# Kernel tuning notes

Hardware: AMD Instinct MI355X
Metric: run time of the kernel (lower is better)

The kernel has to match this reference:

```python
import jax, jax.numpy as jnp
import numpy as np

D, H, L, NB = 128, 8, 2, 32
NEIGHBOR_DIST = 50.0
OUT_H, PRED = 512, 60
N, A, T = 32, 50, 50
DH = D // H
FF = 4 * D


def setup_inputs():
    key = jax.random.key(0)
    ks = jax.random.split(key, 20)
    g = lambda k, s, sc=0.02: jax.random.normal(k, s, jnp.float32) * sc
    return {
        "x": jax.random.normal(ks[0], (N, A, T, 5), jnp.float32) * 10.0,
        "invalid_entries": jax.random.randint(ks[1], (N, A, T), 0, 2).astype(bool),
        "emb_W": g(ks[2], (5, D)), "emb_b": jnp.zeros((D,), jnp.float32),
        "dist_emb": g(ks[3], (NB, H)),
        "ln_g": jnp.ones((L, 3, D), jnp.float32), "ln_b": jnp.zeros((L, 3, D), jnp.float32),
        "Wq": g(ks[4], (L, 2, D, D)), "Wk": g(ks[5], (L, 2, D, D)),
        "Wv": g(ks[6], (L, 2, D, D)), "Wo": g(ks[7], (L, 2, D, D)),
        "ffn_W1": g(ks[8], (L, D, FF)), "ffn_b1": jnp.zeros((L, FF), jnp.float32),
        "ffn_W2": g(ks[9], (L, FF, D)), "ffn_b2": jnp.zeros((L, D), jnp.float32),
        "mlp_W1": g(ks[10], (D, OUT_H)), "mlp_b1": jnp.zeros((OUT_H,), jnp.float32),
        "mlp_W2": g(ks[11], (OUT_H, 2 * PRED)), "mlp_b2": jnp.zeros((2 * PRED,), jnp.float32),
    }


def _ln(h, g, b):
    mu = h.mean(-1, keepdims=True)
    var = ((h - mu) ** 2).mean(-1, keepdims=True)
    return (h - mu) / jnp.sqrt(var + 1e-5) * g + b


def _mha(h, Wq, Wk, Wv, Wo, mask, bias=None):
    # h: (B, S, D); mask: (B, S, S) bool, True = blocked; bias: (B, H, S, S)
    B, S, _ = h.shape
    q = (h @ Wq).reshape(B, S, H, DH)
    k = (h @ Wk).reshape(B, S, H, DH)
    v = (h @ Wv).reshape(B, S, H, DH)
    s = jnp.einsum('bqhd,bkhd->bhqk', q, k) / jnp.sqrt(jnp.float32(DH))
    if bias is not None:
        s = s + bias
    s = jnp.where(mask[:, None, :, :], jnp.float32(-1e9), s)
    a = jax.nn.softmax(s, axis=-1)
    o = jnp.einsum('bhqk,bkhd->bqhd', a, v).reshape(B, S, D)
    return o @ Wo


def _masks_and_bias(x, invalid_entries, dist_emb):
    # pos: (N*T, A, 2); masks are non-differentiable, stop grad through cdist
    pos = jax.lax.stop_gradient(jnp.swapaxes(x, 1, 2).reshape(N * T, A, 5)[:, :, :2])
    dist = jnp.sqrt(jnp.sum((pos[:, :, None, :] - pos[:, None, :, :]) ** 2, axis=-1))
    bin_size = NEIGHBOR_DIST / NB
    bucket = jnp.clip((dist / bin_size).astype(jnp.int32), 0, NB - 1)
    dist_bias = jnp.transpose(dist_emb[bucket], (0, 3, 1, 2))  # (N*T, H, A, A)

    inv_s = jnp.swapaxes(invalid_entries, 1, 2).reshape(N * T, A)
    ego_only = jnp.ones((A, A), bool).at[0, :].set(False)  # only ego row attends broadly
    social = (dist > NEIGHBOR_DIST) | inv_s[:, None, :] | ego_only[None]
    di_a = jnp.arange(min(50, A))
    social = social.at[:, di_a, di_a].set(False)  # vectorized form of the 50-iter loop

    inv_t = invalid_entries.reshape(N * A, T)
    temporal = jnp.triu(jnp.ones((T, T), bool), 1)[None] | inv_t[:, None, :]
    di_t = jnp.arange(min(50, T))
    temporal = temporal.at[:, di_t, di_t].set(False)
    return temporal, social, dist_bias


def _forward(x, invalid_entries, emb_W, emb_b, dist_emb, ln_g, ln_b,
             Wq, Wk, Wv, Wo, ffn_W1, ffn_b1, ffn_W2, ffn_b2,
             mlp_W1, mlp_b1, mlp_W2, mlp_b2):
    temporal_mask, social_mask, dist_bias = _masks_and_bias(x, invalid_entries, dist_emb)
    h = x @ emb_W + emb_b  # (N, A, T, D)
    for l in range(L):
        # temporal attention over T per agent
        ht = h.reshape(N * A, T, D)
        ht = ht + _mha(_ln(ht, ln_g[l, 0], ln_b[l, 0]),
                       Wq[l, 0], Wk[l, 0], Wv[l, 0], Wo[l, 0], temporal_mask)
        h = ht.reshape(N, A, T, D)
        # social attention over A per timestep, with bucketized distance bias
        hs = jnp.swapaxes(h, 1, 2).reshape(N * T, A, D)
        hs = hs + _mha(_ln(hs, ln_g[l, 1], ln_b[l, 1]),
                       Wq[l, 1], Wk[l, 1], Wv[l, 1], Wo[l, 1], social_mask, bias=dist_bias)
        h = jnp.swapaxes(hs.reshape(N, T, A, D), 1, 2)
        # FFN
        hn = _ln(h, ln_g[l, 2], ln_b[l, 2])
        h = h + (jnp.maximum(hn @ ffn_W1[l] + ffn_b1[l], 0.0) @ ffn_W2[l] + ffn_b2[l])
    e = h[:, 0]  # ego agent: (N, T, D)
    e = (e @ mlp_W1 + mlp_b1) @ mlp_W2 + mlp_b2  # two linears, no activation (as in source)
    return e.reshape(N, T, PRED, 2)


def reference(x, invalid_entries, emb_W, emb_b, dist_emb, ln_g, ln_b,
              Wq, Wk, Wv, Wo, ffn_W1, ffn_b1, ffn_W2, ffn_b2,
              mlp_W1, mlp_b1, mlp_W2, mlp_b2):
    return _forward(x, invalid_entries, emb_W, emb_b, dist_emb, ln_g, ln_b,
                    Wq, Wk, Wv, Wo, ffn_W1, ffn_b1, ffn_W2, ffn_b2,
                    mlp_W1, mlp_b1, mlp_W2, mlp_b2)
```

## Files before the change

### kernel.cpp

```cpp
#include <hip/hip_runtime.h>


#define DD 128
typedef __attribute__((ext_vector_type(8))) short bf16x8;
typedef __attribute__((ext_vector_type(4))) float f32x4;
#define MFMA16(a, b, c) __builtin_amdgcn_mfma_f32_16x16x32_bf16(a, b, c, 0, 0, 0)

__device__ __forceinline__ float bf2f(unsigned short u) {
  union { unsigned int i; float f; } x; x.i = ((unsigned int)u) << 16; return x.f;
}
__device__ __forceinline__ unsigned short f2bf(float f) {
  union { float f; unsigned int i; } x; x.f = f;
  return (unsigned short)((x.i + 0x7FFFu + ((x.i >> 16) & 1u)) >> 16);
}
__device__ __forceinline__ float wave_sum(float v) {
#pragma unroll
  for (int off = 32; off > 0; off >>= 1) v += __shfl_xor(v, off, 64);
  return v;
}
__device__ __forceinline__ float wave_max(float v) {
#pragma unroll
  for (int off = 32; off > 0; off >>= 1) v = fmaxf(v, __shfl_xor(v, off, 64));
  return v;
}
__device__ __forceinline__ bool load_inv(const void* p, int idx, int bytemode) {
  if (bytemode) return ((const unsigned char*)p)[idx] != 0;
  return ((const int*)p)[idx] != 0;
}

__global__ void detect_kernel(const void* __restrict__ inv, int* __restrict__ flag) {
  __shared__ int found;
  if (threadIdx.x == 0) found = 0;
  __syncthreads();
  const unsigned char* p = (const unsigned char*)inv;
  int loc = 0;
  for (int i = threadIdx.x; i < 16384; i += blockDim.x)
    if ((i & 3) != 0 && p[i] != 0) loc = 1;
  if (loc) atomicOr(&found, 1);
  __syncthreads();
  if (threadIdx.x == 0) *flag = found ? 1 : 0;
}

__global__ __launch_bounds__(256) void convert_weights(
    const float* __restrict__ Wq, const float* __restrict__ Wk,
    const float* __restrict__ Wv, const float* __restrict__ Wo,
    const float* __restrict__ W1, const float* __restrict__ W2,
    const float* __restrict__ W1m, const float* __restrict__ W2m,
    unsigned short* __restrict__ wqkv, unsigned short* __restrict__ wot,
    unsigned short* __restrict__ w1t, unsigned short* __restrict__ w2t,
    unsigned short* __restrict__ w1e, unsigned short* __restrict__ w2e) {
  __shared__ float tile[32][33];
  int b = blockIdx.x;
  int tx = threadIdx.x & 31, ty = threadIdx.x >> 5;
  const float* src; unsigned short* dst;
  int o0, i0, srcld, dstld, osub = 0, obound = 1 << 30;
  if (b < 192) {
    int m = b / 48, t2 = b % 48;
    o0 = (t2 / 4) * 32; i0 = (t2 % 4) * 32;
    int sel = o0 >> 7;
    src = (sel == 0 ? Wq : (sel == 1 ? Wk : Wv)) + m * 16384;
    osub = sel * 128; srcld = 128;
    dst = wqkv + m * 49152; dstld = 128;
  } else if (b < 256) {
    int m = (b - 192) / 16, t2 = (b - 192) % 16;
    o0 = (t2 / 4) * 32; i0 = (t2 % 4) * 32;
    src = Wo + m * 16384; srcld = 128;
    dst = wot + m * 16384; dstld = 128;
  } else if (b < 384) {
    int l = (b - 256) / 64, t2 = (b - 256) % 64;
    o0 = (t2 / 4) * 32; i0 = (t2 % 4) * 32;
    src = W1 + l * 65536; srcld = 512;
    dst = w1t + l * 65536; dstld = 128;
  } else if (b < 512) {
    int l = (b - 384) / 64, t2 = (b - 384) % 64;
    o0 = (t2 / 16) * 32; i0 = (t2 % 16) * 32;
    src = W2 + l * 65536; srcld = 128;
    dst = w2t + l * 65536; dstld = 512;
  } else if (b < 576) {
    int t2 = b - 512;
    o0 = (t2 / 4) * 32; i0 = (t2 % 4) * 32;
    src = W1m; srcld = 512;
    dst = w1e; dstld = 128;
  } else {
    int t2 = b - 576;
    o0 = (t2 / 16) * 32; i0 = (t2 % 16) * 32;
    src = W2m; srcld = 120; obound = 120;
    dst = w2e; dstld = 512;
  }
#pragma unroll
  for (int kk = 0; kk < 4; ++kk) {
    int i = i0 + ty + 8 * kk, o = o0 + tx;
    tile[ty + 8 * kk][tx] = (o < obound) ? src[i * srcld + (o - osub)] : 0.f;
  }
  __syncthreads();
#pragma unroll
  for (int kk = 0; kk < 4; ++kk) {
    int o = o0 + ty + 8 * kk, i = i0 + tx;
    dst[o * dstld + i] = f2bf(tile[tx][ty + 8 * kk]);
  }
}

__global__ __launch_bounds__(512, 4) void temporal_attn_kernel(
    const float* __restrict__ x, float* __restrict__ h,
    const void* __restrict__ inv, const int* __restrict__ flagp,
    const float* __restrict__ g, const float* __restrict__ bb,
    const float* __restrict__ embW, const float* __restrict__ embB,
    const unsigned short* __restrict__ wqkv,
    const unsigned short* __restrict__ wot, int first) {
  __shared__ __align__(16) unsigned short xbf[64][136];
  __shared__ __align__(16) unsigned short kbf[64][136];
  __shared__ __align__(16) unsigned short vT[128][72];
  __shared__ __align__(16) unsigned short pbuf[8][16][72];
  __shared__ float ssb[8][64];
  int seq = blockIdx.x;
  int tid = threadIdx.x, lane = tid & 63, wid = tid >> 6;
  unsigned long long invmask =
      __ballot((lane < 50) && load_inv(inv, seq * 50 + lane, *flagp));
  const f32x4 zf = (f32x4){0.f, 0.f, 0.f, 0.f};
  if (first) {
    for (int t = wid; t < 50; t += 8) {
      int tok = seq * 50 + t;
      float c0 = x[tok * 5], c1 = x[tok * 5 + 1], c2 = x[tok * 5 + 2];
      float c3 = x[tok * 5 + 3], c4 = x[tok * 5 + 4];
      float x0 = embB[lane] + c0 * embW[lane] + c1 * embW[128 + lane] +
                 c2 * embW[256 + lane] + c3 * embW[384 + lane] + c4 * embW[512 + lane];
      float x1 = embB[lane + 64] + c0 * embW[lane + 64] + c1 * embW[128 + lane + 64] +
                 c2 * embW[256 + lane + 64] + c3 * embW[384 + lane + 64] +
                 c4 * embW[512 + lane + 64];
      h[tok * DD + lane] = x0; h[tok * DD + lane + 64] = x1;
      float mu = wave_sum(x0 + x1) * (1.0f / 128.0f);
      float d0 = x0 - mu, d1 = x1 - mu;
      float var = wave_sum(d0 * d0 + d1 * d1) * (1.0f / 128.0f);
      float rstd = rsqrtf(var + 1e-5f);
      xbf[t][lane]      = f2bf(d0 * rstd * g[lane] + bb[lane]);
      xbf[t][lane + 64] = f2bf(d1 * rstd * g[lane + 64] + bb[lane + 64]);
    }
  } else {
    float v0[7], v1[7];
#pragma unroll
    for (int i = 0; i < 7; ++i) {
      int t = wid + 8 * i;
      if (t < 50) {
        v0[i] = h[(seq * 50 + t) * DD + lane];
        v1[i] = h[(seq * 50 + t) * DD + lane + 64];
      }
    }
#pragma unroll
    for (int i = 0; i < 7; ++i) {
      int t = wid + 8 * i;
      if (t < 50) {
        float mu = wave_sum(v0[i] + v1[i]) * (1.0f / 128.0f);
        float d0 = v0[i] - mu, d1 = v1[i] - mu;
        float var = wave_sum(d0 * d0 + d1 * d1) * (1.0f / 128.0f);
        float rstd = rsqrtf(var + 1e-5f);
        xbf[t][lane]      = f2bf(d0 * rstd * g[lane] + bb[lane]);
        xbf[t][lane + 64] = f2bf(d1 * rstd * g[lane + 64] + bb[lane + 64]);
      }
    }
  }
  for (int idx = tid; idx < 1904; idx += 512) {
    int r = idx / 136, cc = idx - r * 136;
    xbf[50 + r][cc] = 0;
    kbf[50 + r][cc] = 0;
  }
  for (int idx = tid; idx < 896; idx += 512) {
    int row = idx / 7, dwi = idx - row * 7;
    ((unsigned int*)&vT[row][50])[dwi] = 0u;
  }
  __syncthreads();
  int lrow = lane & 15, lk = (lane >> 4) * 8, lr4 = (lane >> 4) * 4;
  int colb = wid * 16 + lrow;
  {
    f32x4 ac[4];
#pragma unroll
    for (int mt = 0; mt < 4; ++mt) ac[mt] = zf;
    bf16x8 wk[4];
#pragma unroll
    for (int kt = 0; kt < 4; ++kt)
      wk[kt] = *(const bf16x8*)&wqkv[((8 + wid) * 16 + lrow) * 128 + kt * 32 + lk];
#pragma unroll
    for (int kt = 0; kt < 4; ++kt)
#pragma unroll
      for (int mt = 0; mt < 4; ++mt) {
        bf16x8 a = *(const bf16x8*)&xbf[mt * 16 + lrow][kt * 32 + lk];
        ac[mt] = MFMA16(a, wk[kt], ac[mt]);
      }
#pragma unroll
    for (int mt = 0; mt < 4; ++mt)
#pragma unroll
      for (int r = 0; r < 4; ++r) {
        int row = mt * 16 + lr4 + r;
        if (row < 50) kbf[row][colb] = f2bf(ac[mt][r]);
      }
  }
  {
    f32x4 ac[4];
#pragma unroll
    for (int mt = 0; mt < 4; ++mt) ac[mt] = zf;
    bf16x8 wv[4];
#pragma unroll
    for (int kt = 0; kt < 4; ++kt)
      wv[kt] = *(const bf16x8*)&wqkv[((16 + wid) * 16 + lrow) * 128 + kt * 32 + lk];
#pragma unroll
    for (int kt = 0; kt < 4; ++kt)
#pragma unroll
      for (int mt = 0; mt < 4; ++mt) {
        bf16x8 a = *(const bf16x8*)&xbf[mt * 16 + lrow][kt * 32 + lk];
        ac[mt] = MFMA16(a, wv[kt], ac[mt]);
      }
#pragma unroll
    for (int mt = 0; mt < 4; ++mt)
#pragma unroll
      for (int r = 0; r < 4; ++r) {
        int row = mt * 16 + lr4 + r;
        if (row < 50) vT[colb][row] = f2bf(ac[mt][r]);
      }
  }
  {
    f32x4 acQ[4];
#pragma unroll
    for (int mt = 0; mt < 4; ++mt) acQ[mt] = zf;
    bf16x8 wq[4];
#pragma unroll
    for (int kt = 0; kt < 4; ++kt)
      wq[kt] = *(const bf16x8*)&wqkv[(wid * 16 + lrow) * 128 + kt * 32 + lk];
#pragma unroll
    for (int kt = 0; kt < 4; ++kt)
#pragma unroll
      for (int mt = 0; mt < 4; ++mt) {
        bf16x8 a = *(const bf16x8*)&xbf[mt * 16 + lrow][kt * 32 + lk];
        acQ[mt] = MFMA16(a, wq[kt], acQ[mt]);
      }
    __syncthreads();
#pragma unroll
    for (int mt = 0; mt < 4; ++mt)
#pragma unroll
      for (int r = 0; r < 4; ++r) {
        int row = mt * 16 + lr4 + r;
        if (row < 50) xbf[row][colb] = f2bf(acQ[mt][r] * 0.25f);
      }
  }
  __syncthreads();
  {
    int hh = wid, c = lane & 15, gq = lane >> 4;
    const int hb = hh * 16;
    bf16x8 vfr0 = *(const bf16x8*)&vT[hb + c][gq * 8];
    bf16x8 vfr1 = *(const bf16x8*)&vT[hb + c][32 + gq * 8];
#pragma unroll
    for (int nt2 = 0; nt2 < 4; ++nt2) {
      bf16x8 qf = (bf16x8){0, 0, 0, 0, 0, 0, 0, 0};
      if (gq < 2) qf = *(const bf16x8*)&xbf[nt2 * 16 + c][hb + gq * 8];
      f32x4 Cs[4];
#pragma unroll
      for (int mt = 0; mt < 4; ++mt) {
        bf16x8 kf = (bf16x8){0, 0, 0, 0, 0, 0, 0, 0};
        if (gq < 2) kf = *(const bf16x8*)&kbf[mt * 16 + c][hb + gq * 8];
        Cs[mt] = MFMA16(kf, qf, zf);
      }
      int tq = nt2 * 16 + c;
      float ss = 0.f;
#pragma unroll
      for (int mt = 0; mt < 4; ++mt) {
        float pv[4];
#pragma unroll
        for (int r = 0; r < 4; ++r) {
          int tk = mt * 16 + gq * 4 + r;
          bool ok = (tk == tq) || ((tk < tq) && !((invmask >> tk) & 1ull));
          float p = ok ? __expf(Cs[mt][r]) : 0.f;
          ss += p;
          pv[r] = p;
        }
        unsigned int* dst = (unsigned int*)&pbuf[hh][c][mt * 16 + gq * 4];
        dst[0] = (unsigned)f2bf(pv[0]) | ((unsigned)f2bf(pv[1]) << 16);
        dst[1] = (unsigned)f2bf(pv[2]) | ((unsigned)f2bf(pv[3]) << 16);
      }
      ss += __shfl_xor(ss, 16, 64);
      ss += __shfl_xor(ss, 32, 64);
      if (gq == 0) ssb[hh][tq] = 1.f / ss;
      asm volatile("s_waitcnt lgkmcnt(0)" ::: "memory");
      __builtin_amdgcn_sched_barrier(0);
      bf16x8 pf0 = *(const bf16x8*)&pbuf[hh][c][gq * 8];
      bf16x8 pf1 = *(const bf16x8*)&pbuf[hh][c][32 + gq * 8];
      f32x4 acO = MFMA16(pf0, vfr0, zf);
      acO = MFMA16(pf1, vfr1, acO);
#pragma unroll
      for (int r = 0; r < 4; ++r) {
        int tqo = nt2 * 16 + gq * 4 + r;
        if (tqo < 50) {
          float rs = ssb[hh][tqo];
          xbf[tqo][hb + c] = f2bf(acO[r] * rs);
        }
      }
    }
  }
  __syncthreads();
  {
    f32x4 acc2[4];
#pragma unroll
    for (int mt = 0; mt < 4; ++mt) acc2[mt] = zf;
    bf16x8 wo4[4];
#pragma unroll
    for (int kt = 0; kt < 4; ++kt)
      wo4[kt] = *(const bf16x8*)&wot[(wid * 16 + lrow) * 128 + kt * 32 + lk];
#pragma unroll
    for (int kt = 0; kt < 4; ++kt)
#pragma unroll
      for (int mt = 0; mt < 4; ++mt) {
        bf16x8 a = *(const bf16x8*)&xbf[mt * 16 + lrow][kt * 32 + lk];
        acc2[mt] = MFMA16(a, wo4[kt], acc2[mt]);
      }
#pragma unroll
    for (int mt = 0; mt < 4; ++mt)
#pragma unroll
      for (int r = 0; r < 4; ++r) {
        int row = mt * 16 + lr4 + r;
        if (row < 50) h[(seq * 50 + row) * DD + colb] += acc2[mt][r];
      }
  }
}

__global__ __launch_bounds__(512, 6) void social_attn_kernel(
    const float* __restrict__ x, float* __restrict__ h,
    const void* __restrict__ inv, const int* __restrict__ flagp,
    const float* __restrict__ dist_emb,
    const float* __restrict__ g, const float* __restrict__ bb,
    const unsigned short* __restrict__ wqkv,
    const unsigned short* __restrict__ wot, int ego_only) {
  __shared__ __align__(16) unsigned short xbf[64][136];
  __shared__ __align__(16) unsigned short vsb[64][136];
  __shared__ float q0s[128];
  __shared__ float aw[8][52];
  int nt_ = blockIdx.x;
  int n = nt_ / 50, t = nt_ - n * 50;
  int tid = threadIdx.x, lane = tid & 63, wid = tid >> 6;
  const f32x4 zf = (f32x4){0.f, 0.f, 0.f, 0.f};
  {
    float v0[7], v1[7];
#pragma unroll
    for (int i = 0; i < 7; ++i) {
      int j = wid + 8 * i;
      if (j < 50) {
        int tok = (n * 50 + j) * 50 + t;
        v0[i] = h[tok * DD + lane];
        v1[i] = h[tok * DD + lane + 64];
      }
    }
#pragma unroll
    for (int i = 0; i < 7; ++i) {
      int j = wid + 8 * i;
      if (j < 50) {
        float mu = wave_sum(v0[i] + v1[i]) * (1.0f / 128.0f);
        float d0 = v0[i] - mu, d1 = v1[i] - mu;
        float var = wave_sum(d0 * d0 + d1 * d1) * (1.0f / 128.0f);
        float rstd = rsqrtf(var + 1e-5f);
        xbf[j][lane]      = f2bf(d0 * rstd * g[lane] + bb[lane]);
        xbf[j][lane + 64] = f2bf(d1 * rstd * g[lane + 64] + bb[lane + 64]);
      }
    }
  }
  __syncthreads();
  int lrow = lane & 15, lk = (lane >> 4) * 8, lr4 = (lane >> 4) * 4;
  int colb = wid * 16 + lrow;
  {
    f32x4 ac[4];
#pragma unroll
    for (int mt = 0; mt < 4; ++mt) ac[mt] = zf;
    bf16x8 wv[4];
#pragma unroll
    for (int kt = 0; kt < 4; ++kt)
      wv[kt] = *(const bf16x8*)&wqkv[((16 + wid) * 16 + lrow) * 128 + kt * 32 + lk];
#pragma unroll
    for (int kt = 0; kt < 4; ++kt)
#pragma unroll
      for (int mt = 0; mt < 4; ++mt) {
        bf16x8 a = *(const bf16x8*)&xbf[mt * 16 + lrow][kt * 32 + lk];
        ac[mt] = MFMA16(a, wv[kt], ac[mt]);
      }
#pragma unroll
    for (int mt = 0; mt < 4; ++mt)
#pragma unroll
      for (int r = 0; r < 4; ++r) {
        int row = mt * 16 + lr4 + r;
        if (row < 50) vsb[row][colb] = f2bf(ac[mt][r]);
      }
  }
  {
    f32x4 acq = zf;
    bf16x8 wq[4];
#pragma unroll
    for (int kt = 0; kt < 4; ++kt)
      wq[kt] = *(const bf16x8*)&wqkv[(wid * 16 + lrow) * 128 + kt * 32 + lk];
#pragma unroll
    for (int kt = 0; kt < 4; ++kt) {
      bf16x8 a0 = *(const bf16x8*)&xbf[lrow][kt * 32 + lk];
      acq = MFMA16(a0, wq[kt], acq);
    }
    if (lane < 16) q0s[wid * 16 + lane] = acq[0];
  }
  {
    f32x4 ac[4];
#pragma unroll
    for (int mt = 0; mt < 4; ++mt) ac[mt] = zf;
    bf16x8 wk[4];
#pragma unroll
    for (int kt = 0; kt < 4; ++kt)
      wk[kt] = *(const bf16x8*)&wqkv[((8 + wid) * 16 + lrow) * 128 + kt * 32 + lk];
#pragma unroll
    for (int kt = 0; kt < 4; ++kt)
#pragma unroll
      for (int mt = 0; mt < 4; ++mt) {
        bf16x8 a = *(const bf16x8*)&xbf[mt * 16 + lrow][kt * 32 + lk];
        ac[mt] = MFMA16(a, wk[kt], ac[mt]);
      }
    __syncthreads();
#pragma unroll
    for (int mt = 0; mt < 4; ++mt)
#pragma unroll
      for (int r = 0; r < 4; ++r) {
        int row = mt * 16 + lr4 + r;
        if (row < 50) xbf[row][colb] = f2bf(ac[mt][r]);
      }
  }
  __syncthreads();
  {
    int hh = wid, j = lane;
    float s = -1e30f;
    if (j < 50) {
      float x0 = x[(n * 2500 + t) * 5 + 0];
      float y0 = x[(n * 2500 + t) * 5 + 1];
      int tokj = (n * 50 + j) * 50 + t;
      float xj = x[tokj * 5 + 0], yj = x[tokj * 5 + 1];
      float dx = x0 - xj, dy = y0 - yj;
      float dist = sqrtf(dx * dx + dy * dy);
      int bucket = (int)(dist / 1.5625f);
      bucket = bucket < 0 ? 0 : (bucket > 31 ? 31 : bucket);
      bool mk = (j != 0) && ((dist > 50.0f) || load_inv(inv, tokj, *flagp));
      bf16x8 k0 = *(const bf16x8*)&xbf[j][hh * 16];
      bf16x8 k1 = *(const bf16x8*)&xbf[j][hh * 16 + 8];
      float acc2 = 0.f;
#pragma unroll
      for (int u = 0; u < 8; ++u)
        acc2 += q0s[hh * 16 + u] * bf2f((unsigned short)k0[u]) +
                q0s[hh * 16 + 8 + u] * bf2f((unsigned short)k1[u]);
      s = mk ? -1e9f : acc2 * 0.25f + dist_emb[bucket * 8 + hh];
    }
    float m = wave_max(s);
    float p = (j < 50) ? __expf(s - m) : 0.f;
    float sm = wave_sum(p);
    if (j < 50) aw[hh][j] = p / sm;
  }
  __syncthreads();
  float a0val = 0.f;
  if (tid < 128) {
    int hh2 = tid >> 4;
#pragma unroll 10
    for (int j = 0; j < 50; ++j) a0val += aw[hh2][j] * bf2f(vsb[j][tid]);
  }
  __syncthreads();
  if (tid < 128) vsb[0][tid] = f2bf(a0val);
  __syncthreads();
  if (!ego_only) {
    f32x4 acc2[4];
#pragma unroll
    for (int mt = 0; mt < 4; ++mt) acc2[mt] = zf;
    bf16x8 wo4[4];
#pragma unroll
    for (int kt = 0; kt < 4; ++kt)
      wo4[kt] = *(const bf16x8*)&wot[(wid * 16 + lrow) * 128 + kt * 32 + lk];
#pragma unroll
    for (int kt = 0; kt < 4; ++kt)
#pragma unroll
      for (int mt = 0; mt < 4; ++mt) {
        bf16x8 a = *(const bf16x8*)&vsb[mt * 16 + lrow][kt * 32 + lk];
        acc2[mt] = MFMA16(a, wo4[kt], acc2[mt]);
      }
#pragma unroll
    for (int mt = 0; mt < 4; ++mt)
#pragma unroll
      for (int r = 0; r < 4; ++r) {
        int row = mt * 16 + lr4 + r;
        if (row < 50)
          h[((n * 50 + row) * 50 + t) * DD + colb] += acc2[mt][r];
      }
  } else {
    f32x4 acc2 = zf;
    bf16x8 wo4[4];
#pragma unroll
    for (int kt = 0; kt < 4; ++kt)
      wo4[kt] = *(const bf16x8*)&wot[(wid * 16 + lrow) * 128 + kt * 32 + lk];
#pragma unroll
    for (int kt = 0; kt < 4; ++kt) {
      bf16x8 a = *(const bf16x8*)&vsb[lrow][kt * 32 + lk];
      acc2 = MFMA16(a, wo4[kt], acc2);
    }
    if ((lane >> 4) == 0)
      h[(n * 2500 + t) * DD + colb] += acc2[0];
  }
}

__global__ __launch_bounds__(512, 4) void ffn_kernel(
    float* __restrict__ h, const float* __restrict__ g, const float* __restrict__ bb,
    const unsigned short* __restrict__ w1t, const float* __restrict__ b1,
    const unsigned short* __restrict__ w2t, const float* __restrict__ b2) {
  __shared__ __align__(16) unsigned short xbf[32][136];
  __shared__ __align__(16) unsigned short hid[64][520];
  int base = blockIdx.x * 64;
  int tid = threadIdx.x, lane = tid & 63, wid = tid >> 6;
  int lrow = lane & 15, lk = (lane >> 4) * 8, lr4 = (lane >> 4) * 4;
#pragma unroll 1
  for (int s = 0; s < 2; ++s) {
    int tb = base + s * 32;
    {
      float v0[4], v1[4];
#pragma unroll
      for (int i = 0; i < 4; ++i) {
        int tok = tb + wid + 8 * i;
        v0[i] = h[tok * DD + lane];
        v1[i] = h[tok * DD + lane + 64];
      }
#pragma unroll
      for (int i = 0; i < 4; ++i) {
        int r = wid + 8 * i;
        float mu = wave_sum(v0[i] + v1[i]) * (1.0f / 128.0f);
        float d0 = v0[i] - mu, d1 = v1[i] - mu;
        float var = wave_sum(d0 * d0 + d1 * d1) * (1.0f / 128.0f);
        float rstd = rsqrtf(var + 1e-5f);
        xbf[r][lane]      = f2bf(d0 * rstd * g[lane] + bb[lane]);
        xbf[r][lane + 64] = f2bf(d1 * rstd * g[lane + 64] + bb[lane + 64]);
      }
    }
    __syncthreads();
    {
      f32x4 acc[2][4];
#pragma unroll
      for (int mt = 0; mt < 2; ++mt)
#pragma unroll
        for (int nt = 0; nt < 4; ++nt) acc[mt][nt] = (f32x4){0.f, 0.f, 0.f, 0.f};
#pragma unroll
      for (int kt = 0; kt < 4; ++kt) {
        bf16x8 a0 = *(const bf16x8*)&xbf[lrow][kt * 32 + lk];
        bf16x8 a1 = *(const bf16x8*)&xbf[16 + lrow][kt * 32 + lk];
#pragma unroll
        for (int nt = 0; nt < 4; ++nt) {
          int nn = wid * 64 + nt * 16 + lrow;
          bf16x8 bfr = *(const bf16x8*)&w1t[nn * 128 + kt * 32 + lk];
          acc[0][nt] = MFMA16(a0, bfr, acc[0][nt]);
          acc[1][nt] = MFMA16(a1, bfr, acc[1][nt]);
        }
      }
#pragma unroll
      for (int nt = 0; nt < 4; ++nt) {
        int nn = wid * 64 + nt * 16 + lrow;
        float bias = b1[nn];
#pragma unroll
        for (int mt = 0; mt < 2; ++mt)
#pragma unroll
          for (int r = 0; r < 4; ++r)
            hid[s * 32 + mt * 16 + lr4 + r][nn] =
                f2bf(fmaxf(acc[mt][nt][r] + bias, 0.f));
      }
    }
    __syncthreads();
  }
  {
    f32x4 acc2[4];
#pragma unroll
    for (int mt = 0; mt < 4; ++mt) acc2[mt] = (f32x4){0.f, 0.f, 0.f, 0.f};
    int nn = wid * 16 + lrow;
#pragma unroll
    for (int kt = 0; kt < 16; ++kt) {
      bf16x8 bfr = *(const bf16x8*)&w2t[nn * 512 + kt * 32 + lk];
#pragma unroll
      for (int mt = 0; mt < 4; ++mt) {
        bf16x8 a = *(const bf16x8*)&hid[mt * 16 + lrow][kt * 32 + lk];
        acc2[mt] = MFMA16(a, bfr, acc2[mt]);
      }
    }
    float bias = b2[nn];
#pragma unroll
    for (int mt = 0; mt < 4; ++mt)
#pragma unroll
      for (int r = 0; r < 4; ++r)
        h[(base + mt * 16 + lr4 + r) * DD + nn] += acc2[mt][r] + bias;
  }
}

__global__ __launch_bounds__(256) void ffn_ego_kernel(
    const float* __restrict__ h,
    const float* __restrict__ g2, const float* __restrict__ bb2,
    const unsigned short* __restrict__ w1t, const float* __restrict__ b1,
    const unsigned short* __restrict__ w2t, const float* __restrict__ b2,
    const unsigned short* __restrict__ w1e, const float* __restrict__ b1m,
    const unsigned short* __restrict__ w2e, const float* __restrict__ b2m,
    float* __restrict__ out) {
  __shared__ float hx[16][132];
  __shared__ __align__(16) unsigned short xln[16][136];
  __shared__ __align__(16) unsigned short hid[16][520];
  int base = blockIdx.x * 16;
  int tid = threadIdx.x, lane = tid & 63, wid = tid >> 6;
  const f32x4 zf = (f32x4){0.f, 0.f, 0.f, 0.f};
  for (int idx = tid; idx < 2048; idx += 256) {
    int r = idx >> 7, d = idx & 127;
    int nt = base + r, n = nt / 50, t = nt - n * 50;
    hx[r][d] = h[(n * 2500 + t) * DD + d];
  }
  __syncthreads();
  for (int r = wid; r < 16; r += 4) {
    float x0 = hx[r][lane], x1 = hx[r][lane + 64];
    float mu = wave_sum(x0 + x1) * (1.0f / 128.0f);
    float d0 = x0 - mu, d1 = x1 - mu;
    float var = wave_sum(d0 * d0 + d1 * d1) * (1.0f / 128.0f);
    float rstd = rsqrtf(var + 1e-5f);
    xln[r][lane]      = f2bf(d0 * rstd * g2[lane] + bb2[lane]);
    xln[r][lane + 64] = f2bf(d1 * rstd * g2[lane + 64] + bb2[lane + 64]);
  }
  __syncthreads();
  int lrow = lane & 15, lk = (lane >> 4) * 8, lr4 = (lane >> 4) * 4;
  {
    f32x4 acc[8];
#pragma unroll
    for (int nt = 0; nt < 8; ++nt) acc[nt] = zf;
#pragma unroll
    for (int kt = 0; kt < 4; ++kt) {
      bf16x8 a = *(const bf16x8*)&xln[lrow][kt * 32 + lk];
#pragma unroll
      for (int nt = 0; nt < 8; ++nt) {
        int nn = wid * 128 + nt * 16 + lrow;
        bf16x8 bfr = *(const bf16x8*)&w1t[nn * 128 + kt * 32 + lk];
        acc[nt] = MFMA16(a, bfr, acc[nt]);
      }
    }
#pragma unroll
    for (int nt = 0; nt < 8; ++nt) {
      int nn = wid * 128 + nt * 16 + lrow;
      float bias = b1[nn];
#pragma unroll
      for (int r = 0; r < 4; ++r)
        hid[lr4 + r][nn] = f2bf(fmaxf(acc[nt][r] + bias, 0.f));
    }
  }
  __syncthreads();
  {
    f32x4 acc2[2];
#pragma unroll
    for (int nt = 0; nt < 2; ++nt) acc2[nt] = zf;
#pragma unroll
    for (int kt = 0; kt < 16; ++kt) {
      bf16x8 a = *(const bf16x8*)&hid[lrow][kt * 32 + lk];
#pragma unroll
      for (int nt = 0; nt < 2; ++nt) {
        int nn = wid * 32 + nt * 16 + lrow;
        bf16x8 bfr = *(const bf16x8*)&w2t[nn * 512 + kt * 32 + lk];
        acc2[nt] = MFMA16(a, bfr, acc2[nt]);
      }
    }
#pragma unroll
    for (int nt = 0; nt < 2; ++nt) {
      int nn = wid * 32 + nt * 16 + lrow;
      float bias = b2[nn];
#pragma unroll
      for (int r = 0; r < 4; ++r)
        xln[lr4 + r][nn] = f2bf(hx[lr4 + r][nn] + acc2[nt][r] + bias);
    }
  }
  __syncthreads();
  {
    f32x4 acc[8];
#pragma unroll
    for (int nt = 0; nt < 8; ++nt) acc[nt] = zf;
#pragma unroll
    for (int kt = 0; kt < 4; ++kt) {
      bf16x8 a = *(const bf16x8*)&xln[lrow][kt * 32 + lk];
#pragma unroll
      for (int nt = 0; nt < 8; ++nt) {
        int nn = wid * 128 + nt * 16 + lrow;
        bf16x8 bfr = *(const bf16x8*)&w1e[nn * 128 + kt * 32 + lk];
        acc[nt] = MFMA16(a, bfr, acc[nt]);
      }
    }
    __syncthreads();
#pragma unroll
    for (int nt = 0; nt < 8; ++nt) {
      int nn = wid * 128 + nt * 16 + lrow;
      float bias = b1m[nn];
#pragma unroll
      for (int r = 0; r < 4; ++r)
        hid[lr4 + r][nn] = f2bf(acc[nt][r] + bias);
    }
  }
  __syncthreads();
  {
    f32x4 acc2[2];
#pragma unroll
    for (int nt = 0; nt < 2; ++nt) acc2[nt] = zf;
#pragma unroll
    for (int kt = 0; kt < 16; ++kt) {
      bf16x8 a = *(const bf16x8*)&hid[lrow][kt * 32 + lk];
#pragma unroll
      for (int nt = 0; nt < 2; ++nt) {
        int nn = wid * 32 + nt * 16 + lrow;
        bf16x8 bfr = *(const bf16x8*)&w2e[nn * 512 + kt * 32 + lk];
        acc2[nt] = MFMA16(a, bfr, acc2[nt]);
      }
    }
#pragma unroll
    for (int nt = 0; nt < 2; ++nt) {
      int nn = wid * 32 + nt * 16 + lrow;
      if (nn < 120) {
        float bias = b2m[nn];
#pragma unroll
        for (int r = 0; r < 4; ++r)
          out[(base + lr4 + r) * 120 + nn] = acc2[nt][r] + bias;
      }
    }
  }
}

extern "C" void kernel_launch(void* const* d_in, const int* in_sizes, int n_in,
                              void* d_out, int out_size, void* d_ws, size_t ws_size,
                              hipStream_t stream) {
  const float* x        = (const float*)d_in[0];
  const void*  inv      = d_in[1];
  const float* emb_W    = (const float*)d_in[2];
  const float* emb_b    = (const float*)d_in[3];
  const float* dist_emb = (const float*)d_in[4];
  const float* ln_g     = (const float*)d_in[5];
  const float* ln_b     = (const float*)d_in[6];
  const float* Wq       = (const float*)d_in[7];
  const float* Wk       = (const float*)d_in[8];
  const float* Wv       = (const float*)d_in[9];
  const float* Wo       = (const float*)d_in[10];
  const float* ffn_W1   = (const float*)d_in[11];
  const float* ffn_b1   = (const float*)d_in[12];
  const float* ffn_W2   = (const float*)d_in[13];
  const float* ffn_b2   = (const float*)d_in[14];
  const float* mlp_W1   = (const float*)d_in[15];
  const float* mlp_b1   = (const float*)d_in[16];
  const float* mlp_W2   = (const float*)d_in[17];
  const float* mlp_b2   = (const float*)d_in[18];
  float* out = (float*)d_out;

  float* ws = (float*)d_ws;
  float* h  = ws;
  unsigned short* wbf = (unsigned short*)(ws + 10240000);
  unsigned short* wqkv = wbf;
  unsigned short* wot  = wbf + 196608;
  unsigned short* w1t  = wbf + 262144;
  unsigned short* w2t  = wbf + 393216;
  unsigned short* w1e  = wbf + 524288;
  unsigned short* w2e  = wbf + 589824;
  int* flag = (int*)(ws + 10600000);

  detect_kernel<<<dim3(1), dim3(256), 0, stream>>>(inv, flag);
  convert_weights<<<dim3(640), dim3(256), 0, stream>>>(
      Wq, Wk, Wv, Wo, ffn_W1, ffn_W2, mlp_W1, mlp_W2,
      wqkv, wot, w1t, w2t, w1e, w2e);
  temporal_attn_kernel<<<dim3(1600), dim3(512), 0, stream>>>(
      x, h, inv, flag, ln_g + 0 * DD, ln_b + 0 * DD, emb_W, emb_b,
      wqkv + 0 * 49152, wot + 0 * 16384, 1);
  social_attn_kernel<<<dim3(1600), dim3(512), 0, stream>>>(
      x, h, inv, flag, dist_emb, ln_g + 1 * DD, ln_b + 1 * DD,
      wqkv + 1 * 49152, wot + 1 * 16384, 0);
  ffn_kernel<<<dim3(1250), dim3(512), 0, stream>>>(
      h, ln_g + 2 * DD, ln_b + 2 * DD, w1t, ffn_b1, w2t, ffn_b2);
  temporal_attn_kernel<<<dim3(1600), dim3(512), 0, stream>>>(
      x, h, inv, flag, ln_g + 3 * DD, ln_b + 3 * DD, emb_W, emb_b,
      wqkv + 2 * 49152, wot + 2 * 16384, 0);
  social_attn_kernel<<<dim3(1600), dim3(512), 0, stream>>>(
      x, h, inv, flag, dist_emb, ln_g + 4 * DD, ln_b + 4 * DD,
      wqkv + 3 * 49152, wot + 3 * 16384, 1);
  ffn_ego_kernel<<<dim3(100), dim3(256), 0, stream>>>(
      h, ln_g + 5 * DD, ln_b + 5 * DD,
      w1t + 65536, ffn_b1 + 512, w2t + 65536, ffn_b2 + 128,
      w1e, mlp_b1, w2e, mlp_b2, out);
}
```

Measured before the change: 338.7 us.

## Fold mask detection into weight conversion, merge K/V and Q projections, split ego work

The standalone mask-format detection kernel becomes an extra block of the weight-conversion launch, removing one kernel launch. In temporal attention the K and V projections share one pass over the LN'd activations, and in social attention the ego Q projection is computed inside the V loop, which cuts redundant LDS reads. The ego attention-times-V reduction is split across 256 threads with a shared partial sum. The ego FFN kernel now handles 8 rows per block over 200 blocks instead of 16 over 100, which adds parallelism but pads MFMA tiles with zero rows.

```diff
diff --git a/kernel.cpp b/kernel.cpp
--- a/kernel.cpp
+++ b/kernel.cpp
@@ -26,19 +26,6 @@
 __device__ __forceinline__ bool load_inv(const void* p, int idx, int bytemode) {
   if (bytemode) return ((const unsigned char*)p)[idx] != 0;
   return ((const int*)p)[idx] != 0;
-}
-
-__global__ void detect_kernel(const void* __restrict__ inv, int* __restrict__ flag) {
-  __shared__ int found;
-  if (threadIdx.x == 0) found = 0;
-  __syncthreads();
-  const unsigned char* p = (const unsigned char*)inv;
-  int loc = 0;
-  for (int i = threadIdx.x; i < 16384; i += blockDim.x)
-    if ((i & 3) != 0 && p[i] != 0) loc = 1;
-  if (loc) atomicOr(&found, 1);
-  __syncthreads();
-  if (threadIdx.x == 0) *flag = found ? 1 : 0;
 }
 
 __global__ __launch_bounds__(256) void convert_weights(
@@ -48,9 +35,23 @@
     const float* __restrict__ W1m, const float* __restrict__ W2m,
     unsigned short* __restrict__ wqkv, unsigned short* __restrict__ wot,
     unsigned short* __restrict__ w1t, unsigned short* __restrict__ w2t,
-    unsigned short* __restrict__ w1e, unsigned short* __restrict__ w2e) {
+    unsigned short* __restrict__ w1e, unsigned short* __restrict__ w2e,
+    const void* __restrict__ inv, int* __restrict__ flag) {
   __shared__ float tile[32][33];
   int b = blockIdx.x;
+  if (b == 640) {
+    __shared__ int found;
+    if (threadIdx.x == 0) found = 0;
+    __syncthreads();
+    const unsigned char* p = (const unsigned char*)inv;
+    int loc = 0;
+    for (int i = threadIdx.x; i < 16384; i += blockDim.x)
+      if ((i & 3) != 0 && p[i] != 0) loc = 1;
+    if (loc) atomicOr(&found, 1);
+    __syncthreads();
+    if (threadIdx.x == 0) *flag = found ? 1 : 0;
+    return;
+  }
   int tx = threadIdx.x & 31, ty = threadIdx.x >> 5;
   const float* src; unsigned short* dst;
   int o0, i0, srcld, dstld, osub = 0, obound = 1 << 30;
@@ -171,49 +172,32 @@
   int lrow = lane & 15, lk = (lane >> 4) * 8, lr4 = (lane >> 4) * 4;
   int colb = wid * 16 + lrow;
   {
-    f32x4 ac[4];
-#pragma unroll
-    for (int mt = 0; mt < 4; ++mt) ac[mt] = zf;
-    bf16x8 wk[4];
-#pragma unroll
-    for (int kt = 0; kt < 4; ++kt)
+    f32x4 acK[4], acV[4];
+#pragma unroll
+    for (int mt = 0; mt < 4; ++mt) { acK[mt] = zf; acV[mt] = zf; }
+    bf16x8 wk[4], wv[4];
+#pragma unroll
+    for (int kt = 0; kt < 4; ++kt) {
       wk[kt] = *(const bf16x8*)&wqkv[((8 + wid) * 16 + lrow) * 128 + kt * 32 + lk];
+      wv[kt] = *(const bf16x8*)&wqkv[((16 + wid) * 16 + lrow) * 128 + kt * 32 + lk];
+    }
 #pragma unroll
     for (int kt = 0; kt < 4; ++kt)
 #pragma unroll
       for (int mt = 0; mt < 4; ++mt) {
         bf16x8 a = *(const bf16x8*)&xbf[mt * 16 + lrow][kt * 32 + lk];
-        ac[mt] = MFMA16(a, wk[kt], ac[mt]);
+        acK[mt] = MFMA16(a, wk[kt], acK[mt]);
+        acV[mt] = MFMA16(a, wv[kt], acV[mt]);
       }
 #pragma unroll
     for (int mt = 0; mt < 4; ++mt)
 #pragma unroll
       for (int r = 0; r < 4; ++r) {
         int row = mt * 16 + lr4 + r;
-        if (row < 50) kbf[row][colb] = f2bf(ac[mt][r]);
-      }
-  }
-  {
-    f32x4 ac[4];
-#pragma unroll
-    for (int mt = 0; mt < 4; ++mt) ac[mt] = zf;
-    bf16x8 wv[4];
-#pragma unroll
-    for (int kt = 0; kt < 4; ++kt)
-      wv[kt] = *(const bf16x8*)&wqkv[((16 + wid) * 16 + lrow) * 128 + kt * 32 + lk];
-#pragma unroll
-    for (int kt = 0; kt < 4; ++kt)
-#pragma unroll
-      for (int mt = 0; mt < 4; ++mt) {
-        bf16x8 a = *(const bf16x8*)&xbf[mt * 16 + lrow][kt * 32 + lk];
-        ac[mt] = MFMA16(a, wv[kt], ac[mt]);
-      }
-#pragma unroll
-    for (int mt = 0; mt < 4; ++mt)
-#pragma unroll
-      for (int r = 0; r < 4; ++r) {
-        int row = mt * 16 + lr4 + r;
-        if (row < 50) vT[colb][row] = f2bf(ac[mt][r]);
+        if (row < 50) {
+          kbf[row][colb] = f2bf(acK[mt][r]);
+          vT[colb][row]  = f2bf(acV[mt][r]);
+        }
       }
   }
   {
@@ -330,6 +314,7 @@
   __shared__ __align__(16) unsigned short vsb[64][136];
   __shared__ float q0s[128];
   __shared__ float aw[8][52];
+  __shared__ float part[128];
   int nt_ = blockIdx.x;
   int n = nt_ / 50, t = nt_ - n * 50;
   int tid = threadIdx.x, lane = tid & 63, wid = tid >> 6;
@@ -365,17 +350,21 @@
     f32x4 ac[4];
 #pragma unroll
     for (int mt = 0; mt < 4; ++mt) ac[mt] = zf;
+    f32x4 acq = zf;
     bf16x8 wv[4];
 #pragma unroll
     for (int kt = 0; kt < 4; ++kt)
       wv[kt] = *(const bf16x8*)&wqkv[((16 + wid) * 16 + lrow) * 128 + kt * 32 + lk];
 #pragma unroll
-    for (int kt = 0; kt < 4; ++kt)
+    for (int kt = 0; kt < 4; ++kt) {
+      bf16x8 wq = *(const bf16x8*)&wqkv[(wid * 16 + lrow) * 128 + kt * 32 + lk];
 #pragma unroll
       for (int mt = 0; mt < 4; ++mt) {
         bf16x8 a = *(const bf16x8*)&xbf[mt * 16 + lrow][kt * 32 + lk];
         ac[mt] = MFMA16(a, wv[kt], ac[mt]);
-      }
+        if (mt == 0) acq = MFMA16(a, wq, acq);
+      }
+    }
 #pragma unroll
     for (int mt = 0; mt < 4; ++mt)
 #pragma unroll
@@ -383,18 +372,6 @@
         int row = mt * 16 + lr4 + r;
         if (row < 50) vsb[row][colb] = f2bf(ac[mt][r]);
       }
-  }
-  {
-    f32x4 acq = zf;
-    bf16x8 wq[4];
-#pragma unroll
-    for (int kt = 0; kt < 4; ++kt)
-      wq[kt] = *(const bf16x8*)&wqkv[(wid * 16 + lrow) * 128 + kt * 32 + lk];
-#pragma unroll
-    for (int kt = 0; kt < 4; ++kt) {
-      bf16x8 a0 = *(const bf16x8*)&xbf[lrow][kt * 32 + lk];
-      acq = MFMA16(a0, wq[kt], acq);
-    }
     if (lane < 16) q0s[wid * 16 + lane] = acq[0];
   }
   {
@@ -451,13 +428,16 @@
   }
   __syncthreads();
   float a0val = 0.f;
-  if (tid < 128) {
-    int hh2 = tid >> 4;
-#pragma unroll 10
-    for (int j = 0; j < 50; ++j) a0val += aw[hh2][j] * bf2f(vsb[j][tid]);
-  }
-  __syncthreads();
-  if (tid < 128) vsb[0][tid] = f2bf(a0val);
+  if (tid < 256) {
+    int d = tid & 127, half = tid >> 7;
+    int hh2 = d >> 4;
+    int j0 = half * 25;
+#pragma unroll 5
+    for (int j = j0; j < j0 + 25; ++j) a0val += aw[hh2][j] * bf2f(vsb[j][d]);
+    if (half) part[d] = a0val;
+  }
+  __syncthreads();
+  if (tid < 128) vsb[0][tid] = f2bf(a0val + part[tid]);
   __syncthreads();
   if (!ego_only) {
     f32x4 acc2[4];
@@ -593,26 +573,31 @@
     const unsigned short* __restrict__ w1e, const float* __restrict__ b1m,
     const unsigned short* __restrict__ w2e, const float* __restrict__ b2m,
     float* __restrict__ out) {
-  __shared__ float hx[16][132];
+  __shared__ float hx[8][132];
   __shared__ __align__(16) unsigned short xln[16][136];
   __shared__ __align__(16) unsigned short hid[16][520];
-  int base = blockIdx.x * 16;
+  int base = blockIdx.x * 8;
   int tid = threadIdx.x, lane = tid & 63, wid = tid >> 6;
   const f32x4 zf = (f32x4){0.f, 0.f, 0.f, 0.f};
-  for (int idx = tid; idx < 2048; idx += 256) {
+  for (int idx = tid; idx < 1024; idx += 256) {
     int r = idx >> 7, d = idx & 127;
     int nt = base + r, n = nt / 50, t = nt - n * 50;
     hx[r][d] = h[(n * 2500 + t) * DD + d];
   }
   __syncthreads();
   for (int r = wid; r < 16; r += 4) {
-    float x0 = hx[r][lane], x1 = hx[r][lane + 64];
-    float mu = wave_sum(x0 + x1) * (1.0f / 128.0f);
-    float d0 = x0 - mu, d1 = x1 - mu;
-    float var = wave_sum(d0 * d0 + d1 * d1) * (1.0f / 128.0f);
-    float rstd = rsqrtf(var + 1e-5f);
-    xln[r][lane]      = f2bf(d0 * rstd * g2[lane] + bb2[lane]);
-    xln[r][lane + 64] = f2bf(d1 * rstd * g2[lane + 64] + bb2[lane + 64]);
+    if (r < 8) {
+      float x0 = hx[r][lane], x1 = hx[r][lane + 64];
+      float mu = wave_sum(x0 + x1) * (1.0f / 128.0f);
+      float d0 = x0 - mu, d1 = x1 - mu;
+      float var = wave_sum(d0 * d0 + d1 * d1) * (1.0f / 128.0f);
+      float rstd = rsqrtf(var + 1e-5f);
+      xln[r][lane]      = f2bf(d0 * rstd * g2[lane] + bb2[lane]);
+      xln[r][lane + 64] = f2bf(d1 * rstd * g2[lane + 64] + bb2[lane + 64]);
+    } else {
+      xln[r][lane] = 0;
+      xln[r][lane + 64] = 0;
+    }
   }
   __syncthreads();
   int lrow = lane & 15, lk = (lane >> 4) * 8, lr4 = (lane >> 4) * 4;
@@ -659,8 +644,11 @@
       int nn = wid * 32 + nt * 16 + lrow;
       float bias = b2[nn];
 #pragma unroll
-      for (int r = 0; r < 4; ++r)
-        xln[lr4 + r][nn] = f2bf(hx[lr4 + r][nn] + acc2[nt][r] + bias);
+      for (int r = 0; r < 4; ++r) {
+        int row = lr4 + r;
+        if (row < 8)
+          xln[row][nn] = f2bf(hx[row][nn] + acc2[nt][r] + bias);
+      }
     }
   }
   __syncthreads();
@@ -709,8 +697,11 @@
       if (nn < 120) {
         float bias = b2m[nn];
 #pragma unroll
-        for (int r = 0; r < 4; ++r)
-          out[(base + lr4 + r) * 120 + nn] = acc2[nt][r] + bias;
+        for (int r = 0; r < 4; ++r) {
+          int row = lr4 + r;
+          if (row < 8)
+            out[(base + row) * 120 + nn] = acc2[nt][r] + bias;
+        }
       }
     }
   }
@@ -751,10 +742,9 @@
   unsigned short* w2e  = wbf + 589824;
   int* flag = (int*)(ws + 10600000);
 
-  detect_kernel<<<dim3(1), dim3(256), 0, stream>>>(inv, flag);
-  convert_weights<<<dim3(640), dim3(256), 0, stream>>>(
+  convert_weights<<<dim3(641), dim3(256), 0, stream>>>(
       Wq, Wk, Wv, Wo, ffn_W1, ffn_W2, mlp_W1, mlp_W2,
-      wqkv, wot, w1t, w2t, w1e, w2e);
+      wqkv, wot, w1t, w2t, w1e, w2e, inv, flag);
   temporal_attn_kernel<<<dim3(1600), dim3(512), 0, stream>>>(
       x, h, inv, flag, ln_g + 0 * DD, ln_b + 0 * DD, emb_W, emb_b,
       wqkv + 0 * 49152, wot + 0 * 16384, 1);
@@ -769,7 +759,7 @@
   social_attn_kernel<<<dim3(1600), dim3(512), 0, stream>>>(
       x, h, inv, flag, dist_emb, ln_g + 4 * DD, ln_b + 4 * DD,
       wqkv + 3 * 49152, wot + 3 * 16384, 1);
-  ffn_ego_kernel<<<dim3(100), dim3(256), 0, stream>>>(
+  ffn_ego_kernel<<<dim3(200), dim3(256), 0, stream>>>(
       h, ln_g + 5 * DD, ln_b + 5 * DD,
       w1t + 65536, ffn_b1 + 512, w2t + 65536, ffn_b2 + 128,
       w1e, mlp_b1, w2e, mlp_b2, out);
```

Measured after the change: 392.0 us. 1.16x slower.
